# Kernel optimization log

Measured on AMD Instinct MI355X. Metric: run time of the kernel, lower is better.

The kernel has to match this reference:

```python
import jax, jax.numpy as jnp
import numpy as np

TAU = 1.0            # temperature (self.temperature.item())
FAST_WEIGHT_DECAY = 0.01
FAST_WEIGHT_LR = 0.01

B, IN, H = 128, 1024, 1024


def setup_inputs() -> dict:
    key = jax.random.key(0)
    k = jax.random.split(key, 6)
    scale_ih = 1.0 / np.sqrt(IN)
    scale_hh = np.sqrt(2.0 / (H + H))  # xavier_uniform-like std
    return {
        "x_t": jax.random.normal(k[0], (B, IN), jnp.float32),
        "h_prev": jax.random.normal(k[1], (B, H), jnp.float32),
        "W_ih": jax.random.normal(k[2], (H, IN), jnp.float32) * scale_ih,
        "b_ih": jnp.zeros((H,), jnp.float32),
        "W_hh_fixed": jax.random.normal(k[3], (H, H), jnp.float32) * scale_hh,
        "W_hh_virtual": jnp.zeros((H, H), jnp.float32),
        "gumbel_u": jax.random.uniform(k[4], (B, H, H), jnp.float32),
    }


def reference(x_t, h_prev, W_ih, b_ih, W_hh_fixed, W_hh_virtual, gumbel_u):
    # input contribution: Linear(input_size, hidden_size)
    input_contrib = x_t @ W_ih.T + b_ih                      # (B, H)

    # logits scaled by temperature once, then gumbel_softmax divides by tau again
    logits = (W_hh_fixed + W_hh_virtual) / TAU               # (H, H)
    eps = 1e-9
    g = -jnp.log(-jnp.log(jnp.clip(gumbel_u, eps, 1.0 - eps)))  # Gumbel(0,1), (B,H,H)
    y = jax.nn.softmax((logits[None, :, :] + g) / TAU, axis=2)  # soft sampling, (B,H,H)

    # weighted exchange: each output neuron o reduces sampled weights against h_prev
    contrib = jnp.einsum('boh,bh->bo', y, h_prev)            # (B, H)
    h_next = jnp.tanh(input_contrib + contrib)               # (B, H)

    # Hebbian fast-weight update (no_grad in original)
    hebbian = jnp.einsum('bo,bh->oh', h_next, h_prev) / B    # mean over batch, (H,H)
    W_hh_virtual_new = jax.lax.stop_gradient(
        W_hh_virtual * (1.0 - FAST_WEIGHT_DECAY) + hebbian * FAST_WEIGHT_LR
    )
    return h_next, W_hh_virtual_new
```

## Files before the change

### kernel.cpp

```cpp
#include <hip/hip_runtime.h>
#include <hip/hip_bf16.h>
#include <cstddef>

#define B_DIM  128
#define IN_DIM 1024
#define H_DIM  1024

constexpr float kDecay   = 1.0f - 0.01f;
constexpr float kLrOverB = 0.01f / 128.0f;

__global__ __launch_bounds__(256) void input_gemm(
    const float* __restrict__ x_t,
    const float* __restrict__ W_ih,
    const float* __restrict__ b_ih,
    float* __restrict__ ic)
{
    const int o0 = blockIdx.x * 64;
    const int b0 = blockIdx.y * 16;
    const int t  = threadIdx.x;

    __shared__ float Wt[64][68];
    __shared__ float xs[64][17];

    const int tx = t & 15;
    const int ty = t >> 4;

    float acc[4] = {0.f, 0.f, 0.f, 0.f};

    for (int kc = 0; kc < IN_DIM / 64; ++kc) {
        const int k0 = kc * 64;

#pragma unroll
        for (int ii = 0; ii < 4; ++ii) {
            const int i  = t + 256 * ii;
            const int r  = i >> 4;
            const int c4 = (i & 15) * 4;
            const float4 wv = *reinterpret_cast<const float4*>(
                &W_ih[(size_t)(o0 + r) * IN_DIM + k0 + c4]);
            Wt[c4 + 0][r] = wv.x; Wt[c4 + 1][r] = wv.y;
            Wt[c4 + 2][r] = wv.z; Wt[c4 + 3][r] = wv.w;
        }
        {
            const int br = t >> 4;
            const int c4 = (t & 15) * 4;
            const float4 xv = *reinterpret_cast<const float4*>(
                &x_t[(size_t)(b0 + br) * IN_DIM + k0 + c4]);
            xs[c4 + 0][br] = xv.x; xs[c4 + 1][br] = xv.y;
            xs[c4 + 2][br] = xv.z; xs[c4 + 3][br] = xv.w;
        }
        __syncthreads();

#pragma unroll 8
        for (int k = 0; k < 64; ++k) {
            const float  xb = xs[k][ty];
            const float4 wv = *reinterpret_cast<const float4*>(&Wt[k][4 * tx]);
            acc[0] = fmaf(wv.x, xb, acc[0]);
            acc[1] = fmaf(wv.y, xb, acc[1]);
            acc[2] = fmaf(wv.z, xb, acc[2]);
            acc[3] = fmaf(wv.w, xb, acc[3]);
        }
        __syncthreads();
    }

    const int o = o0 + 4 * tx;
    const int b = b0 + ty;
    float4 r;
    r.x = acc[0] + b_ih[o + 0];
    r.y = acc[1] + b_ih[o + 1];
    r.z = acc[2] + b_ih[o + 2];
    r.w = acc[3] + b_ih[o + 3];
    *reinterpret_cast<float4*>(&ic[(size_t)b * H_DIM + o]) = r;
}

__global__ __launch_bounds__(512, 4) void fused_rows(
    const float* __restrict__ h_prev,
    const float* __restrict__ W_f,
    const float* __restrict__ W_v,
    const float* __restrict__ gu,
    const float* __restrict__ ic,
    float* __restrict__ h_next)
{
    const int o0 = blockIdx.x * 8;
    const int b0 = blockIdx.y * 8;
    const int t  = threadIdx.x;

    __shared__ __align__(16) float el[8 * H_DIM];

#pragma unroll
    for (int ii = 0; ii < 4; ++ii) {
        const int i = t + 512 * ii;
        const int r = i >> 8;
        const int c = i & 255;
        const size_t off = (size_t)(o0 + r) * H_DIM + 4 * c;
        const float4 a = *reinterpret_cast<const float4*>(W_f + off);
        const float4 b = *reinterpret_cast<const float4*>(W_v + off);
        float4 e;
        e.x = __expf(a.x + b.x); e.y = __expf(a.y + b.y);
        e.z = __expf(a.z + b.z); e.w = __expf(a.w + b.w);
        reinterpret_cast<float4*>(el)[i] = e;
    }
    __syncthreads();

    const int w = t >> 6, lane = t & 63;
    const int b = b0 + w;

    const float4* hp4 = reinterpret_cast<const float4*>(h_prev + (size_t)b * H_DIM);
    float4 hp[4];
#pragma unroll
    for (int j = 0; j < 4; ++j) hp[j] = hp4[lane + 64 * j];

    const float4* el4 = reinterpret_cast<const float4*>(el);

#pragma unroll 2
    for (int oi = 0; oi < 8; ++oi) {
        const int o = o0 + oi;
        const float4* g4 =
            reinterpret_cast<const float4*>(gu + ((size_t)b * H_DIM + o) * H_DIM);

        float sum = 0.f, dot = 0.f;
#pragma unroll
        for (int j = 0; j < 4; ++j) {
            const float4 u = g4[lane + 64 * j];
            const float4 e = el4[oi * 256 + lane + 64 * j];
            const float4 p = hp[j];

            const float t0 = -__logf(fmaxf(u.x, 1e-9f));
            const float t1 = -__logf(fmaxf(u.y, 1e-9f));
            const float t2 = -__logf(fmaxf(u.z, 1e-9f));
            const float t3 = -__logf(fmaxf(u.w, 1e-9f));
            const float q0 = __fdividef(e.x, t0);
            const float q1 = __fdividef(e.y, t1);
            const float q2 = __fdividef(e.z, t2);
            const float q3 = __fdividef(e.w, t3);
            sum += q0 + q1 + q2 + q3;
            dot = fmaf(q0, p.x, dot);
            dot = fmaf(q1, p.y, dot);
            dot = fmaf(q2, p.z, dot);
            dot = fmaf(q3, p.w, dot);
        }

#pragma unroll
        for (int off = 32; off > 0; off >>= 1) {
            sum += __shfl_xor(sum, off, 64);
            dot += __shfl_xor(dot, off, 64);
        }

        if (lane == 0) {
            h_next[(size_t)b * H_DIM + o] =
                tanhf(ic[(size_t)b * H_DIM + o] + dot / sum);
        }
    }
}

__global__ __launch_bounds__(256) void hebbian_update(
    const float* __restrict__ h_next,
    const float* __restrict__ h_prev,
    const float* __restrict__ W_v,
    float* __restrict__ W_out)
{
    const int h0 = blockIdx.x * 64;
    const int o0 = blockIdx.y * 64;
    const int t  = threadIdx.x;

    __shared__ __align__(16) float hn_s[B_DIM][64];
    __shared__ __align__(16) float hp_s[B_DIM][64];

#pragma unroll
    for (int i = 0; i < 32; ++i) {
        const int e  = t + 256 * i;
        const int bb = e >> 6;
        const int cc = e & 63;
        hn_s[bb][cc] = h_next[(size_t)bb * H_DIM + o0 + cc];
        hp_s[bb][cc] = h_prev[(size_t)bb * H_DIM + h0 + cc];
    }
    __syncthreads();

    const int tx = t & 15;
    const int ty = t >> 4;

    float acc[4][4] = {{0.f}};

#pragma unroll 8
    for (int b = 0; b < B_DIM; ++b) {
        const float4 av = reinterpret_cast<const float4*>(hn_s[b])[ty];
        const float4 bv = reinterpret_cast<const float4*>(hp_s[b])[tx];
        const float aa[4] = {av.x, av.y, av.z, av.w};
        const float bb[4] = {bv.x, bv.y, bv.z, bv.w};
#pragma unroll
        for (int a = 0; a < 4; ++a)
#pragma unroll
            for (int c = 0; c < 4; ++c)
                acc[a][c] = fmaf(aa[a], bb[c], acc[a][c]);
    }

#pragma unroll
    for (int a = 0; a < 4; ++a) {
        const int o = o0 + 4 * ty + a;
        const size_t base = (size_t)o * H_DIM + h0 + 4 * tx;
        const float4 wv = *reinterpret_cast<const float4*>(W_v + base);
        float4 r;
        r.x = wv.x * kDecay + acc[a][0] * kLrOverB;
        r.y = wv.y * kDecay + acc[a][1] * kLrOverB;
        r.z = wv.z * kDecay + acc[a][2] * kLrOverB;
        r.w = wv.w * kDecay + acc[a][3] * kLrOverB;
        *reinterpret_cast<float4*>(W_out + base) = r;
    }
}

extern "C" void kernel_launch(void* const* d_in, const int* in_sizes, int n_in,
                              void* d_out, int out_size, void* d_ws, size_t ws_size,
                              hipStream_t stream)
{
    const float* x_t    = (const float*)d_in[0];
    const float* h_prev = (const float*)d_in[1];
    const float* W_ih   = (const float*)d_in[2];
    const float* b_ih   = (const float*)d_in[3];
    const float* W_f    = (const float*)d_in[4];
    const float* W_v    = (const float*)d_in[5];
    const float* gu     = (const float*)d_in[6];

    float* out    = (float*)d_out;
    float* h_next = out;
    float* W_out  = out + (size_t)B_DIM * H_DIM;
    float* ic     = (float*)d_ws;

    input_gemm<<<dim3(H_DIM / 64, B_DIM / 16), 256, 0, stream>>>(
        x_t, W_ih, b_ih, ic);

    fused_rows<<<dim3(H_DIM / 8, B_DIM / 8), 512, 0, stream>>>(
        h_prev, W_f, W_v, gu, ic, h_next);

    hebbian_update<<<dim3(H_DIM / 64, H_DIM / 64), 256, 0, stream>>>(
        h_next, h_prev, W_v, W_out);
}
```

Measured before the change: 168.0 us.

## Precompute exp logits once and stream them from global in fused row kernel

Adds a separate kernel that computes exp(W_f + W_v) once into workspace, instead of every block recomputing eight rows into shared memory. The fused row kernel now maps one batch per block row, with each wave handling eight outputs. Each wave unrolls all eight rows to keep more loads in flight, batches the shuffle reductions, and stores results as vectors. It also uses log2 instead of ln, which is safe because the constant factor cancels in dot/sum. The trade-off is that the exp matrix is re-read from L2/MALL for every batch rather than held in LDS, which adds cache traffic.

Measured after the change: 162.1 us. 3.5% less time.

```diff
diff --git a/kernel.cpp b/kernel.cpp
--- a/kernel.cpp
+++ b/kernel.cpp
@@ -8,6 +8,20 @@
 
 constexpr float kDecay   = 1.0f - 0.01f;
 constexpr float kLrOverB = 0.01f / 128.0f;
+
+__global__ __launch_bounds__(256) void exp_logits(
+    const float* __restrict__ W_f,
+    const float* __restrict__ W_v,
+    float* __restrict__ E)
+{
+    const int i = blockIdx.x * 256 + threadIdx.x;
+    const float4 a = reinterpret_cast<const float4*>(W_f)[i];
+    const float4 b = reinterpret_cast<const float4*>(W_v)[i];
+    float4 e;
+    e.x = __expf(a.x + b.x); e.y = __expf(a.y + b.y);
+    e.z = __expf(a.z + b.z); e.w = __expf(a.w + b.w);
+    reinterpret_cast<float4*>(E)[i] = e;
+}
 
 __global__ __launch_bounds__(256) void input_gemm(
     const float* __restrict__ x_t,
@@ -72,83 +86,78 @@
     *reinterpret_cast<float4*>(&ic[(size_t)b * H_DIM + o]) = r;
 }
 
-__global__ __launch_bounds__(512, 4) void fused_rows(
+__global__ __launch_bounds__(256) void fused_rows(
     const float* __restrict__ h_prev,
-    const float* __restrict__ W_f,
-    const float* __restrict__ W_v,
+    const float* __restrict__ E,
     const float* __restrict__ gu,
     const float* __restrict__ ic,
     float* __restrict__ h_next)
 {
-    const int o0 = blockIdx.x * 8;
-    const int b0 = blockIdx.y * 8;
-    const int t  = threadIdx.x;
-
-    __shared__ __align__(16) float el[8 * H_DIM];
-
-#pragma unroll
-    for (int ii = 0; ii < 4; ++ii) {
-        const int i = t + 512 * ii;
-        const int r = i >> 8;
-        const int c = i & 255;
-        const size_t off = (size_t)(o0 + r) * H_DIM + 4 * c;
-        const float4 a = *reinterpret_cast<const float4*>(W_f + off);
-        const float4 b = *reinterpret_cast<const float4*>(W_v + off);
-        float4 e;
-        e.x = __expf(a.x + b.x); e.y = __expf(a.y + b.y);
-        e.z = __expf(a.z + b.z); e.w = __expf(a.w + b.w);
-        reinterpret_cast<float4*>(el)[i] = e;
-    }
-    __syncthreads();
-
-    const int w = t >> 6, lane = t & 63;
-    const int b = b0 + w;
+    const int b    = blockIdx.y;
+    const int t    = threadIdx.x;
+    const int w    = t >> 6;
+    const int lane = t & 63;
+    const int ob   = blockIdx.x * 32 + w * 8;
 
     const float4* hp4 = reinterpret_cast<const float4*>(h_prev + (size_t)b * H_DIM);
     float4 hp[4];
 #pragma unroll
     for (int j = 0; j < 4; ++j) hp[j] = hp4[lane + 64 * j];
 
-    const float4* el4 = reinterpret_cast<const float4*>(el);
-
-#pragma unroll 2
-    for (int oi = 0; oi < 8; ++oi) {
-        const int o = o0 + oi;
-        const float4* g4 =
-            reinterpret_cast<const float4*>(gu + ((size_t)b * H_DIM + o) * H_DIM);
-
+    const float4* g4 = reinterpret_cast<const float4*>(gu + ((size_t)b * H_DIM + ob) * H_DIM);
+    const float4* e4 = reinterpret_cast<const float4*>(E + (size_t)ob * H_DIM);
+
+    float s[8], d[8];
+
+#pragma unroll
+    for (int r = 0; r < 8; ++r) {
         float sum = 0.f, dot = 0.f;
 #pragma unroll
         for (int j = 0; j < 4; ++j) {
-            const float4 u = g4[lane + 64 * j];
-            const float4 e = el4[oi * 256 + lane + 64 * j];
+            const int idx = r * 256 + lane + 64 * j;
+            const float4 u = g4[idx];
+            const float4 e = e4[idx];
             const float4 p = hp[j];
 
-            const float t0 = -__logf(fmaxf(u.x, 1e-9f));
-            const float t1 = -__logf(fmaxf(u.y, 1e-9f));
-            const float t2 = -__logf(fmaxf(u.z, 1e-9f));
-            const float t3 = -__logf(fmaxf(u.w, 1e-9f));
-            const float q0 = __fdividef(e.x, t0);
-            const float q1 = __fdividef(e.y, t1);
-            const float q2 = __fdividef(e.z, t2);
-            const float q3 = __fdividef(e.w, t3);
-            sum += q0 + q1 + q2 + q3;
+            const float q0 = __fdividef(e.x, -__log2f(fmaxf(u.x, 1e-9f)));
+            const float q1 = __fdividef(e.y, -__log2f(fmaxf(u.y, 1e-9f)));
+            const float q2 = __fdividef(e.z, -__log2f(fmaxf(u.z, 1e-9f)));
+            const float q3 = __fdividef(e.w, -__log2f(fmaxf(u.w, 1e-9f)));
+
+            sum += (q0 + q1) + (q2 + q3);
             dot = fmaf(q0, p.x, dot);
             dot = fmaf(q1, p.y, dot);
             dot = fmaf(q2, p.z, dot);
             dot = fmaf(q3, p.w, dot);
         }
-
-#pragma unroll
-        for (int off = 32; off > 0; off >>= 1) {
-            sum += __shfl_xor(sum, off, 64);
-            dot += __shfl_xor(dot, off, 64);
-        }
-
-        if (lane == 0) {
-            h_next[(size_t)b * H_DIM + o] =
-                tanhf(ic[(size_t)b * H_DIM + o] + dot / sum);
-        }
+        s[r] = sum;
+        d[r] = dot;
+    }
+
+#pragma unroll
+    for (int off = 32; off > 0; off >>= 1) {
+#pragma unroll
+        for (int r = 0; r < 8; ++r) {
+            s[r] += __shfl_xor(s[r], off, 64);
+            d[r] += __shfl_xor(d[r], off, 64);
+        }
+    }
+
+    if (lane == 0) {
+        const size_t base = (size_t)b * H_DIM + ob;
+        const float4 i0 = *reinterpret_cast<const float4*>(ic + base);
+        const float4 i1 = *reinterpret_cast<const float4*>(ic + base + 4);
+        float4 r0, r1;
+        r0.x = tanhf(i0.x + __fdividef(d[0], s[0]));
+        r0.y = tanhf(i0.y + __fdividef(d[1], s[1]));
+        r0.z = tanhf(i0.z + __fdividef(d[2], s[2]));
+        r0.w = tanhf(i0.w + __fdividef(d[3], s[3]));
+        r1.x = tanhf(i1.x + __fdividef(d[4], s[4]));
+        r1.y = tanhf(i1.y + __fdividef(d[5], s[5]));
+        r1.z = tanhf(i1.z + __fdividef(d[6], s[6]));
+        r1.w = tanhf(i1.w + __fdividef(d[7], s[7]));
+        *reinterpret_cast<float4*>(h_next + base)     = r0;
+        *reinterpret_cast<float4*>(h_next + base + 4) = r1;
     }
 }
 
@@ -222,13 +231,17 @@
     float* out    = (float*)d_out;
     float* h_next = out;
     float* W_out  = out + (size_t)B_DIM * H_DIM;
-    float* ic     = (float*)d_ws;
+
+    float* E  = (float*)d_ws;
+    float* ic = E + (size_t)H_DIM * H_DIM;
+
+    exp_logits<<<dim3(H_DIM * H_DIM / 1024), 256, 0, stream>>>(W_f, W_v, E);
 
     input_gemm<<<dim3(H_DIM / 64, B_DIM / 16), 256, 0, stream>>>(
         x_t, W_ih, b_ih, ic);
 
-    fused_rows<<<dim3(H_DIM / 8, B_DIM / 8), 512, 0, stream>>>(
-        h_prev, W_f, W_v, gu, ic, h_next);
+    fused_rows<<<dim3(H_DIM / 32, B_DIM), 256, 0, stream>>>(
+        h_prev, E, gu, ic, h_next);
 
     hebbian_update<<<dim3(H_DIM / 64, H_DIM / 64), 256, 0, stream>>>(
         h_next, h_prev, W_v, W_out);
```
